# Kernel optimization log

Measured on AMD Instinct MI355X. Metric: run time of the kernel, lower is better.

The kernel has to match this reference:

```python
import jax, jax.numpy as jnp
import numpy as np

N = 100000
E = 1600000


def _sage_conv(x, src, tgt, W_l, b, W_r):
    # PyG SAGEConv (mean aggr): out = lin_l(mean_{j in N(i)} x_j) + lin_r(x_i)
    msg = x[src]                                            # [E, F] gather
    agg = jax.ops.segment_sum(msg, tgt, num_segments=N)     # [N, F]
    deg = jax.ops.segment_sum(jnp.ones((src.shape[0],), x.dtype), tgt, num_segments=N)
    agg = agg / jnp.maximum(deg, 1.0)[:, None]               # mean
    return agg @ W_l + b + x @ W_r


def setup_inputs() -> dict:
    key = jax.random.key(0)
    ks = jax.random.split(key, 16)
    d = {
        "x": jax.random.normal(ks[0], (N, 9), jnp.float32),
        "edge_index": jax.random.randint(ks[1], (2, E), 0, N, jnp.int32).astype(jnp.int64),
        "W1_l": jax.random.normal(ks[2], (9, 128), jnp.float32) / np.sqrt(9),
        "b1": jnp.zeros((128,), jnp.float32),
        "W1_r": jax.random.normal(ks[3], (9, 128), jnp.float32) / np.sqrt(9),
        "W2_l": jax.random.normal(ks[4], (128, 128), jnp.float32) / np.sqrt(128),
        "b2": jnp.zeros((128,), jnp.float32),
        "W2_r": jax.random.normal(ks[5], (128, 128), jnp.float32) / np.sqrt(128),
        "W3_l": jax.random.normal(ks[6], (128, 128), jnp.float32) / np.sqrt(128),
        "b3": jnp.zeros((128,), jnp.float32),
        "W3_r": jax.random.normal(ks[7], (128, 128), jnp.float32) / np.sqrt(128),
        "Wl1": jax.random.normal(ks[8], (128, 128), jnp.float32) / np.sqrt(128),
        "bl1": jnp.zeros((128,), jnp.float32),
        "Wl2": jax.random.normal(ks[9], (128, 64), jnp.float32) / np.sqrt(128),
        "bl2": jnp.zeros((64,), jnp.float32),
        "Wl3": jax.random.normal(ks[10], (64, 3), jnp.float32) / np.sqrt(64),
        "bl3": jnp.zeros((3,), jnp.float32),
    }
    return d


def reference(x, edge_index, W1_l, b1, W1_r, W2_l, b2, W2_r, W3_l, b3, W3_r,
              Wl1, bl1, Wl2, bl2, Wl3, bl3):
    src, tgt = edge_index[0], edge_index[1]
    h = jax.nn.relu(_sage_conv(x, src, tgt, W1_l, b1, W1_r))   # dropout = identity (eval)
    h = jax.nn.relu(_sage_conv(h, src, tgt, W2_l, b2, W2_r))
    h = jax.nn.relu(_sage_conv(h, src, tgt, W3_l, b3, W3_r))
    h = jax.nn.relu(h @ Wl1 + bl1)
    h = jax.nn.relu(h @ Wl2 + bl2)
    h = h @ Wl3 + bl3
    return jax.nn.log_softmax(h, axis=-1)
```

## Files before the change

### kernel.cpp

```cpp
#include <hip/hip_runtime.h>
#include <hip/hip_fp16.h>
#include <stdint.h>

typedef _Float16 f16x8 __attribute__((ext_vector_type(8)));
typedef float f32x4 __attribute__((ext_vector_type(4)));


#define CH 2048
#define MAXNB 1024

__global__ __launch_bounds__(256) void bhist_k(const int* __restrict__ ei,
        int* __restrict__ bh, int E, int shift, int NB, int NBLK) {
    __shared__ int lh[MAXNB];
    for (int b = threadIdx.x; b < NB; b += 256) lh[b] = 0;
    __syncthreads();
    int base = blockIdx.x * CH;
    int end = min(base + CH, E);
    for (int e = base + threadIdx.x; e < end; e += 256) {
        int t = ei[(size_t)E + e];
        atomicAdd(&lh[t >> shift], 1);
    }
    __syncthreads();
    for (int b = threadIdx.x; b < NB; b += 256)
        bh[(size_t)b * NBLK + blockIdx.x] = lh[b];
}

__global__ __launch_bounds__(256) void scan_col_k(int* bh, int* __restrict__ btot,
                                                  int NBLK, int NB) {
    __shared__ int sd[256];
    size_t rowoff = (size_t)blockIdx.x * NBLK;
    int t = threadIdx.x;
    int base = t * 4;
    int v0 = (base + 0 < NBLK) ? bh[rowoff + base + 0] : 0;
    int v1 = (base + 1 < NBLK) ? bh[rowoff + base + 1] : 0;
    int v2 = (base + 2 < NBLK) ? bh[rowoff + base + 2] : 0;
    int v3 = (base + 3 < NBLK) ? bh[rowoff + base + 3] : 0;
    int s = v0 + v1 + v2 + v3;
    sd[t] = s;
    __syncthreads();
    for (int off = 1; off < 256; off <<= 1) {
        int x = (t >= off) ? sd[t - off] : 0;
        __syncthreads();
        sd[t] += x;
        __syncthreads();
    }
    int ex = sd[t] - s;
    if (base + 0 < NBLK) bh[rowoff + base + 0] = ex;
    if (base + 1 < NBLK) bh[rowoff + base + 1] = ex + v0;
    if (base + 2 < NBLK) bh[rowoff + base + 2] = ex + v0 + v1;
    if (base + 3 < NBLK) bh[rowoff + base + 3] = ex + v0 + v1 + v2;
    if (t == 255) btot[blockIdx.x] = sd[255];
}

__global__ void scan_block_k(const int* __restrict__ deg, int* __restrict__ excl,
                             int* __restrict__ bsum, int N) {
    __shared__ int sd[256];
    int t = threadIdx.x;
    int base = blockIdx.x * 1024 + t * 4;
    int v0 = (base + 0 < N) ? deg[base + 0] : 0;
    int v1 = (base + 1 < N) ? deg[base + 1] : 0;
    int v2 = (base + 2 < N) ? deg[base + 2] : 0;
    int v3 = (base + 3 < N) ? deg[base + 3] : 0;
    int s = v0 + v1 + v2 + v3;
    sd[t] = s;
    __syncthreads();
    for (int off = 1; off < 256; off <<= 1) {
        int x = (t >= off) ? sd[t - off] : 0;
        __syncthreads();
        sd[t] += x;
        __syncthreads();
    }
    int incl = sd[t];
    int ex = incl - s;
    if (base + 0 < N) excl[base + 0] = ex;
    if (base + 1 < N) excl[base + 1] = ex + v0;
    if (base + 2 < N) excl[base + 2] = ex + v0 + v1;
    if (base + 3 < N) excl[base + 3] = ex + v0 + v1 + v2;
    if (t == 255) bsum[blockIdx.x] = incl;
}

__global__ __launch_bounds__(256) void bscatter_k(const int* __restrict__ ei,
        const int* __restrict__ bh, const int* __restrict__ bbase,
        int* __restrict__ staged, int E, int shift, int NB, int NBLK) {
    __shared__ int cur[MAXNB];
    for (int b = threadIdx.x; b < NB; b += 256)
        cur[b] = bbase[b] + bh[(size_t)b * NBLK + blockIdx.x];
    __syncthreads();
    int base = blockIdx.x * CH;
    int end = min(base + CH, E);
    int mask = (1 << shift) - 1;
    for (int e = base + threadIdx.x; e < end; e += 256) {
        int s = ei[e];
        int t = ei[(size_t)E + e];
        int p = atomicAdd(&cur[t >> shift], 1);
        staged[p] = s | ((t & mask) << 17);
    }
}

__global__ __launch_bounds__(256) void csrfill_k(const int* __restrict__ staged,
        const int* __restrict__ bbase, int* __restrict__ rs, int* __restrict__ csr,
        int N, int E, int shift, int NB) {
    __shared__ int lh[256];
    __shared__ int sd[256];
    int b = blockIdx.x;
    int tpb = 1 << shift;
    int t0 = b << shift;
    int s0 = bbase[b];
    int s1 = (b == NB - 1) ? E : bbase[b + 1];
    int t = threadIdx.x;
    if (t < tpb) lh[t] = 0;
    __syncthreads();
    for (int e = s0 + t; e < s1; e += 256)
        atomicAdd(&lh[staged[e] >> 17], 1);
    __syncthreads();
    int v = (t < tpb) ? lh[t] : 0;
    sd[t] = v;
    __syncthreads();
    for (int off = 1; off < 256; off <<= 1) {
        int x = (t >= off) ? sd[t - off] : 0;
        __syncthreads();
        sd[t] += x;
        __syncthreads();
    }
    if (t < tpb) {
        int excl = sd[t] - v;
        lh[t] = excl;
        int tg = t0 + t;
        if (tg < N) rs[tg] = s0 + excl;
    }
    if (b == NB - 1 && t == 0) rs[N] = E;
    __syncthreads();
    for (int e = s0 + t; e < s1; e += 256) {
        int w = staged[e];
        int lt = w >> 17;
        int src = w & 0x1FFFF;
        int p = s0 + atomicAdd(&lh[lt], 1);
        csr[p] = src;
    }
}


__global__ void xcast_k(const float* __restrict__ x, __half* __restrict__ x16,
                        int N) {
    int i = blockIdx.x * blockDim.x + threadIdx.x;
    if (i >= N) return;
    const float* xr = x + (size_t)i * 9;
    union { _Float16 h[16]; uint4 u4[2]; } o;
    #pragma unroll
    for (int f = 0; f < 9; ++f) o.h[f] = (_Float16)xr[f];
    #pragma unroll
    for (int f = 9; f < 16; ++f) o.h[f] = (_Float16)0.f;
    uint4* dst = reinterpret_cast<uint4*>(x16 + (size_t)i * 16);
    dst[0] = o.u4[0];
    dst[1] = o.u4[1];
}

__global__ void agg9pack_k(const __half* __restrict__ x16, const int* __restrict__ rs,
                           const int* __restrict__ csr, __half* __restrict__ a32,
                           int N) {
    int i = blockIdx.x * blockDim.x + threadIdx.x;
    if (i >= N) return;
    int s0 = rs[i], s1 = rs[i + 1];
    const uint4* h4 = reinterpret_cast<const uint4*>(x16);
    float a[9];
    #pragma unroll
    for (int f = 0; f < 9; ++f) a[f] = 0.f;
    auto acc9 = [&](int src) {
        uint4 va = h4[(size_t)src * 2];
        unsigned int wb = *reinterpret_cast<const unsigned int*>(
            x16 + (size_t)src * 16 + 8);
        const __half2* p = reinterpret_cast<const __half2*>(&va);
        #pragma unroll
        for (int q = 0; q < 4; ++q) {
            float2 f = __half22float2(p[q]);
            a[q * 2]     += f.x;
            a[q * 2 + 1] += f.y;
        }
        __half2 h8 = *reinterpret_cast<const __half2*>(&wb);
        a[8] += __half22float2(h8).x;
    };
    int j = s0;
    for (; j + 2 <= s1; j += 2) { acc9(csr[j]); acc9(csr[j + 1]); }
    if (j < s1) acc9(csr[j]);
    float inv = (s1 > s0) ? 1.f / (float)(s1 - s0) : 0.f;
    union { _Float16 h[32]; uint4 u4[4]; } o;
    #pragma unroll
    for (int f = 0; f < 9; ++f) o.h[f] = (_Float16)(a[f] * inv);
    const _Float16* sx = reinterpret_cast<const _Float16*>(x16 + (size_t)i * 16);
    #pragma unroll
    for (int f = 0; f < 9; ++f) o.h[9 + f] = sx[f];
    #pragma unroll
    for (int f = 18; f < 32; ++f) o.h[f] = (_Float16)0.f;
    uint4* dst = reinterpret_cast<uint4*>(a32 + (size_t)i * 32);
    #pragma unroll
    for (int q = 0; q < 4; ++q) dst[q] = o.u4[q];
}

__global__ __launch_bounds__(256) void agg128h4_k(const __half* __restrict__ h16,
        const int* __restrict__ rs, const int* __restrict__ csr,
        __half* __restrict__ out, int N) {
    int l16 = threadIdx.x & 15;
    int node = blockIdx.x * 16 + (threadIdx.x >> 4);
    if (node >= N) return;
    int s0 = rs[node], s1 = rs[node + 1];
    const uint4* h4 = reinterpret_cast<const uint4*>(h16);
    float acc[8];
    #pragma unroll
    for (int c = 0; c < 8; ++c) acc[c] = 0.f;
    int j = s0;
    for (; j + 4 <= s1; j += 4) {
        uint4 v[4];
        #pragma unroll
        for (int u = 0; u < 4; ++u)
            v[u] = h4[(size_t)csr[j + u] * 16 + l16];
        #pragma unroll
        for (int u = 0; u < 4; ++u) {
            const __half2* p = reinterpret_cast<const __half2*>(&v[u]);
            #pragma unroll
            for (int q = 0; q < 4; ++q) {
                float2 f = __half22float2(p[q]);
                acc[q * 2]     += f.x;
                acc[q * 2 + 1] += f.y;
            }
        }
    }
    for (; j < s1; ++j) {
        uint4 vv = h4[(size_t)csr[j] * 16 + l16];
        const __half2* p = reinterpret_cast<const __half2*>(&vv);
        #pragma unroll
        for (int q = 0; q < 4; ++q) {
            float2 f = __half22float2(p[q]);
            acc[q * 2]     += f.x;
            acc[q * 2 + 1] += f.y;
        }
    }
    float inv = (s1 > s0) ? 1.f / (float)(s1 - s0) : 0.f;
    __half2 o[4];
    #pragma unroll
    for (int q = 0; q < 4; ++q)
        o[q] = __floats2half2_rn(acc[q * 2] * inv, acc[q * 2 + 1] * inv);
    reinterpret_cast<uint4*>(out)[(size_t)node * 16 + l16] =
        *reinterpret_cast<uint4*>(o);
}


struct WPD { const float* W; _Float16* dst; int K, N; };
struct WPD6 { WPD d[6]; };

__global__ void wpack6_k(WPD6 all) {
    WPD w = all.d[blockIdx.y];
    int idx = blockIdx.x * blockDim.x + threadIdx.x;
    int kcb = w.K / 32;
    int total = (w.N / 16) * kcb * 64;
    if (idx >= total) return;
    int lane = idx & 63;
    int blk = idx >> 6;
    int kb = blk % kcb;
    int nf = blk / kcb;
    int col = nf * 16 + (lane & 15);
    int k0 = kb * 32 + (lane >> 4) * 8;
    f16x8 v;
    #pragma unroll
    for (int j = 0; j < 8; ++j)
        v[j] = (_Float16)w.W[(size_t)(k0 + j) * w.N + col];
    *reinterpret_cast<f16x8*>(w.dst + (size_t)idx * 8) = v;
}

__global__ void wpack1_k(const float* __restrict__ Wl, const float* __restrict__ Wr,
                         _Float16* __restrict__ wpk) {
    int idx = blockIdx.x * blockDim.x + threadIdx.x;
    if (idx >= 8 * 64) return;
    int lane = idx & 63;
    int nf = idx >> 6;
    int col = nf * 16 + (lane & 15);
    int k0 = (lane >> 4) * 8;
    f16x8 v;
    #pragma unroll
    for (int j = 0; j < 8; ++j) {
        int k = k0 + j;
        float w = (k < 9) ? Wl[(size_t)k * 128 + col]
                : (k < 18) ? Wr[(size_t)(k - 9) * 128 + col] : 0.f;
        v[j] = (_Float16)w;
    }
    *reinterpret_cast<f16x8*>(wpk + (size_t)idx * 8) = v;
}

template<int NF, int NS, int KK>
__global__ __launch_bounds__(256) void mfma_lin_k(
        const __half* A1, const __half* A2,
        const _Float16* __restrict__ pk1, const _Float16* __restrict__ pk2,
        const float* __restrict__ bias, __half* C, int M) {
    constexpr int TN = 64 * NF;
    constexpr int KB = KK / 32;
    constexpr int LPR = KK / 8;
    constexpr int RPI = 256 / LPR;
    constexpr int ITER = 64 / RPI;
    __shared__ _Float16 a_lds[NS][64][KK + 8];

    int tid = threadIdx.x;
    int lane = tid & 63;
    int wave = tid >> 6;
    int rb = blockIdx.x * 64;

    const __half* As[2] = {A1, A2};
    #pragma unroll
    for (int s = 0; s < NS; ++s) {
        #pragma unroll
        for (int i = 0; i < ITER; ++i) {
            int row = (tid / LPR) + i * RPI;
            int c = tid % LPR;
            int grow = rb + row;
            uint4 v = make_uint4(0, 0, 0, 0);
            if (grow < M)
                v = reinterpret_cast<const uint4*>(As[s] + (size_t)grow * KK)[c];
            *reinterpret_cast<uint4*>(&a_lds[s][row][c * 8]) = v;
        }
    }

    const _Float16* pks[2] = {pk1, pk2};
    f16x8 bfrag[NS][KB][NF];
    #pragma unroll
    for (int s = 0; s < NS; ++s)
        #pragma unroll
        for (int kb = 0; kb < KB; ++kb)
            #pragma unroll
            for (int n = 0; n < NF; ++n) {
                int nf = wave * NF + n;
                bfrag[s][kb][n] =
                    reinterpret_cast<const f16x8*>(pks[s])[(size_t)(nf * KB + kb) * 64 + lane];
            }

    f32x4 acc[4][NF];
    #pragma unroll
    for (int m = 0; m < 4; ++m)
        #pragma unroll
        for (int n = 0; n < NF; ++n)
            acc[m][n] = (f32x4){0.f, 0.f, 0.f, 0.f};

    __syncthreads();

    #pragma unroll
    for (int s = 0; s < NS; ++s)
        #pragma unroll
        for (int kb = 0; kb < KB; ++kb)
            #pragma unroll
            for (int m = 0; m < 4; ++m) {
                f16x8 a = *reinterpret_cast<const f16x8*>(
                    &a_lds[s][m * 16 + (lane & 15)][kb * 32 + (lane >> 4) * 8]);
                #pragma unroll
                for (int n = 0; n < NF; ++n)
                    acc[m][n] = __builtin_amdgcn_mfma_f32_16x16x32_f16(
                        a, bfrag[s][kb][n], acc[m][n], 0, 0, 0);
            }

    #pragma unroll
    for (int n = 0; n < NF; ++n) {
        int col = wave * NF * 16 + n * 16 + (lane & 15);
        float bv = bias[col];
        #pragma unroll
        for (int m = 0; m < 4; ++m) {
            #pragma unroll
            for (int j = 0; j < 4; ++j) {
                int grow = rb + m * 16 + (lane >> 4) * 4 + j;
                if (grow < M) {
                    float v = fmaxf(acc[m][n][j] + bv, 0.f);
                    C[(size_t)grow * TN + col] = __float2half_rn(v);
                }
            }
        }
    }
}

__global__ __launch_bounds__(256) void mfma_lin_final_k(
        const __half* A1, const _Float16* __restrict__ pk1,
        const float* __restrict__ bias,
        const float* __restrict__ W3, const float* __restrict__ b3,
        float* __restrict__ outp, int M) {
    constexpr int KK = 128;
    __shared__ _Float16 a_lds[64][136];
    __shared__ float smem[64][68];

    int tid = threadIdx.x;
    int lane = tid & 63;
    int wave = tid >> 6;
    int rb = blockIdx.x * 64;

    #pragma unroll
    for (int i = 0; i < 4; ++i) {
        int row = (tid >> 4) + i * 16;
        int grow = rb + row;
        uint4 v = make_uint4(0, 0, 0, 0);
        if (grow < M)
            v = reinterpret_cast<const uint4*>(A1 + (size_t)grow * KK)[tid & 15];
        *reinterpret_cast<uint4*>(&a_lds[row][(tid & 15) * 8]) = v;
    }

    f16x8 bfrag[4];
    #pragma unroll
    for (int kb = 0; kb < 4; ++kb)
        bfrag[kb] = reinterpret_cast<const f16x8*>(pk1)[(size_t)(wave * 4 + kb) * 64 + lane];

    f32x4 acc[4];
    #pragma unroll
    for (int m = 0; m < 4; ++m) acc[m] = (f32x4){0.f, 0.f, 0.f, 0.f};

    __syncthreads();

    #pragma unroll
    for (int kb = 0; kb < 4; ++kb)
        #pragma unroll
        for (int m = 0; m < 4; ++m) {
            f16x8 a = *reinterpret_cast<const f16x8*>(
                &a_lds[m * 16 + (lane & 15)][kb * 32 + (lane >> 4) * 8]);
            acc[m] = __builtin_amdgcn_mfma_f32_16x16x32_f16(a, bfrag[kb], acc[m], 0, 0, 0);
        }

    int col = wave * 16 + (lane & 15);
    float bv = bias[col];
    #pragma unroll
    for (int m = 0; m < 4; ++m)
        #pragma unroll
        for (int j = 0; j < 4; ++j) {
            int row = m * 16 + (lane >> 4) * 4 + j;
            smem[row][col] = fmaxf(acc[m][j] + bv, 0.f);
        }
    __syncthreads();

    if (tid < 64) {
        int grow = rb + tid;
        if (grow < M) {
            float l0 = b3[0], l1 = b3[1], l2 = b3[2];
            #pragma unroll 8
            for (int k = 0; k < 64; ++k) {
                float v = smem[tid][k];
                l0 = fmaf(v, W3[k * 3 + 0], l0);
                l1 = fmaf(v, W3[k * 3 + 1], l1);
                l2 = fmaf(v, W3[k * 3 + 2], l2);
            }
            float mx = fmaxf(l0, fmaxf(l1, l2));
            float e0 = expf(l0 - mx), e1 = expf(l1 - mx), e2 = expf(l2 - mx);
            float lse = logf(e0 + e1 + e2) + mx;
            outp[(size_t)grow * 3 + 0] = l0 - lse;
            outp[(size_t)grow * 3 + 1] = l1 - lse;
            outp[(size_t)grow * 3 + 2] = l2 - lse;
        }
    }
}


extern "C" void kernel_launch(void* const* d_in, const int* in_sizes, int n_in,
                              void* d_out, int out_size, void* d_ws, size_t ws_size,
                              hipStream_t stream) {
    const float* x   = (const float*)d_in[0];
    const int* ei    = (const int*)d_in[1];
    const float* W1l = (const float*)d_in[2];
    const float* b1  = (const float*)d_in[3];
    const float* W1r = (const float*)d_in[4];
    const float* W2l = (const float*)d_in[5];
    const float* b2  = (const float*)d_in[6];
    const float* W2r = (const float*)d_in[7];
    const float* W3l = (const float*)d_in[8];
    const float* b3  = (const float*)d_in[9];
    const float* W3r = (const float*)d_in[10];
    const float* Wl1 = (const float*)d_in[11];
    const float* bl1 = (const float*)d_in[12];
    const float* Wl2 = (const float*)d_in[13];
    const float* bl2 = (const float*)d_in[14];
    const float* Wl3 = (const float*)d_in[15];
    const float* bl3 = (const float*)d_in[16];
    float* out = (float*)d_out;

    const int N = in_sizes[0] / 9;
    const int E = in_sizes[1] / 2;

    char* ws = (char*)d_ws;
    size_t off = 0;
    auto alloc = [&](size_t bytes) -> void* {
        void* p = ws + off;
        off += (bytes + 255) & ~(size_t)255;
        return p;
    };
    __half* h16    = (__half*)alloc((size_t)N * 128 * sizeof(__half));
    __half* agg16  = (__half*)alloc((size_t)N * 128 * sizeof(__half));
    __half* a32    = (__half*)alloc((size_t)N * 32 * sizeof(__half));
    __half* x16    = (__half*)alloc((size_t)N * 16 * sizeof(__half));
    int* rs     = (int*)alloc((size_t)(N + 1) * sizeof(int));
    int* csr    = (int*)alloc((size_t)E * sizeof(int));
    int* staged = (int*)alloc((size_t)E * sizeof(int));
    _Float16* wpk1  = (_Float16*)alloc(32 * 128 * sizeof(_Float16));
    _Float16* wpk2l = (_Float16*)alloc(128 * 128 * sizeof(_Float16));
    _Float16* wpk2r = (_Float16*)alloc(128 * 128 * sizeof(_Float16));
    _Float16* wpk3l = (_Float16*)alloc(128 * 128 * sizeof(_Float16));
    _Float16* wpk3r = (_Float16*)alloc(128 * 128 * sizeof(_Float16));
    _Float16* wpkl1 = (_Float16*)alloc(128 * 128 * sizeof(_Float16));
    _Float16* wpkl2 = (_Float16*)alloc(128 * 64 * sizeof(_Float16));
    (void)ws_size; (void)n_in; (void)out_size;

    int shift = 7;
    while ((((size_t)N + ((size_t)1 << shift) - 1) >> shift) > MAXNB) ++shift;
    const int NB = (N + (1 << shift) - 1) >> shift;
    const int NBLK = (E + CH - 1) / CH;
    int* bh    = (int*)alloc((size_t)NB * NBLK * sizeof(int));
    int* btot  = (int*)alloc((size_t)NB * sizeof(int));
    int* bbase = (int*)alloc((size_t)(NB + 1) * sizeof(int));
    int* bsum  = (int*)alloc(64 * sizeof(int));

    WPD6 wp;
    wp.d[0] = {W2l, wpk2l, 128, 128};
    wp.d[1] = {W2r, wpk2r, 128, 128};
    wp.d[2] = {W3l, wpk3l, 128, 128};
    wp.d[3] = {W3r, wpk3r, 128, 128};
    wp.d[4] = {Wl1, wpkl1, 128, 128};
    wp.d[5] = {Wl2, wpkl2, 128, 64};
    wpack6_k<<<dim3(8, 6), 256, 0, stream>>>(wp);
    wpack1_k<<<2, 256, 0, stream>>>(W1l, W1r, wpk1);
    xcast_k<<<(N + 255) / 256, 256, 0, stream>>>(x, x16, N);

    bhist_k<<<NBLK, 256, 0, stream>>>(ei, bh, E, shift, NB, NBLK);
    scan_col_k<<<NB, 256, 0, stream>>>(bh, btot, NBLK, NB);
    scan_block_k<<<1, 256, 0, stream>>>(btot, bbase, bsum, NB);
    bscatter_k<<<NBLK, 256, 0, stream>>>(ei, bh, bbase, staged, E, shift, NB, NBLK);
    csrfill_k<<<NB, 256, 0, stream>>>(staged, bbase, rs, csr, N, E, shift, NB);

    const int gemm_grid = (N + 63) / 64;
    const int agg_grid = (N + 15) / 16;

    agg9pack_k<<<(N + 255) / 256, 256, 0, stream>>>(x16, rs, csr, a32, N);
    mfma_lin_k<2, 1, 32><<<gemm_grid, 256, 0, stream>>>(
        a32, nullptr, wpk1, nullptr, b1, h16, N);

    agg128h4_k<<<agg_grid, 256, 0, stream>>>(h16, rs, csr, agg16, N);
    mfma_lin_k<2, 2, 128><<<gemm_grid, 256, 0, stream>>>(
        agg16, h16, wpk2l, wpk2r, b2, h16, N);

    agg128h4_k<<<agg_grid, 256, 0, stream>>>(h16, rs, csr, agg16, N);
    mfma_lin_k<2, 2, 128><<<gemm_grid, 256, 0, stream>>>(
        agg16, h16, wpk3l, wpk3r, b3, h16, N);

    mfma_lin_k<2, 1, 128><<<gemm_grid, 256, 0, stream>>>(
        h16, nullptr, wpkl1, nullptr, bl1, h16, N);
    mfma_lin_final_k<<<gemm_grid, 256, 0, stream>>>(
        h16, wpkl2, bl2, Wl3, bl3, out, N);
}
```

Baseline: 289.6 us.

## Fuse neighbor mean aggregation into SAGE layer GEMM kernel

Replaces the separate 128-wide gather-mean kernel and the following MFMA GEMM with a single kernel. Each block aggregates neighbors for its 64 rows directly into LDS, loads its own rows into a second LDS buffer, then runs both weight products from LDS. This removes the write and re-read of the intermediate aggregate buffer and one launch per layer. Because a node's output now depends on other blocks' inputs, it ping-pongs between two feature buffers, and each block now does gather and GEMM in sequence, which can lower occupancy and overlap.

```diff
diff --git a/kernel.cpp b/kernel.cpp
--- a/kernel.cpp
+++ b/kernel.cpp
@@ -194,53 +194,6 @@
     uint4* dst = reinterpret_cast<uint4*>(a32 + (size_t)i * 32);
     #pragma unroll
     for (int q = 0; q < 4; ++q) dst[q] = o.u4[q];
-}
-
-__global__ __launch_bounds__(256) void agg128h4_k(const __half* __restrict__ h16,
-        const int* __restrict__ rs, const int* __restrict__ csr,
-        __half* __restrict__ out, int N) {
-    int l16 = threadIdx.x & 15;
-    int node = blockIdx.x * 16 + (threadIdx.x >> 4);
-    if (node >= N) return;
-    int s0 = rs[node], s1 = rs[node + 1];
-    const uint4* h4 = reinterpret_cast<const uint4*>(h16);
-    float acc[8];
-    #pragma unroll
-    for (int c = 0; c < 8; ++c) acc[c] = 0.f;
-    int j = s0;
-    for (; j + 4 <= s1; j += 4) {
-        uint4 v[4];
-        #pragma unroll
-        for (int u = 0; u < 4; ++u)
-            v[u] = h4[(size_t)csr[j + u] * 16 + l16];
-        #pragma unroll
-        for (int u = 0; u < 4; ++u) {
-            const __half2* p = reinterpret_cast<const __half2*>(&v[u]);
-            #pragma unroll
-            for (int q = 0; q < 4; ++q) {
-                float2 f = __half22float2(p[q]);
-                acc[q * 2]     += f.x;
-                acc[q * 2 + 1] += f.y;
-            }
-        }
-    }
-    for (; j < s1; ++j) {
-        uint4 vv = h4[(size_t)csr[j] * 16 + l16];
-        const __half2* p = reinterpret_cast<const __half2*>(&vv);
-        #pragma unroll
-        for (int q = 0; q < 4; ++q) {
-            float2 f = __half22float2(p[q]);
-            acc[q * 2]     += f.x;
-            acc[q * 2 + 1] += f.y;
-        }
-    }
-    float inv = (s1 > s0) ? 1.f / (float)(s1 - s0) : 0.f;
-    __half2 o[4];
-    #pragma unroll
-    for (int q = 0; q < 4; ++q)
-        o[q] = __floats2half2_rn(acc[q * 2] * inv, acc[q * 2 + 1] * inv);
-    reinterpret_cast<uint4*>(out)[(size_t)node * 16 + l16] =
-        *reinterpret_cast<uint4*>(o);
 }
 
 
@@ -365,6 +318,130 @@
                 if (grow < M) {
                     float v = fmaxf(acc[m][n][j] + bv, 0.f);
                     C[(size_t)grow * TN + col] = __float2half_rn(v);
+                }
+            }
+        }
+    }
+}
+
+__global__ __launch_bounds__(256) void agg_gemm_k(
+        const __half* __restrict__ hin,
+        const int* __restrict__ rs, const int* __restrict__ csr,
+        const _Float16* __restrict__ pkl, const _Float16* __restrict__ pkr,
+        const float* __restrict__ bias, __half* __restrict__ hout, int M) {
+    constexpr int KK = 128;
+    __shared__ _Float16 a_lds[2][64][KK + 8];
+
+    int tid = threadIdx.x;
+    int lane = tid & 63;
+    int wave = tid >> 6;
+    int rb = blockIdx.x * 64;
+    int l16 = lane & 15;
+
+    #pragma unroll
+    for (int i = 0; i < 4; ++i) {
+        int row = (tid >> 4) + i * 16;
+        int grow = rb + row;
+        uint4 v = make_uint4(0, 0, 0, 0);
+        if (grow < M)
+            v = reinterpret_cast<const uint4*>(hin + (size_t)grow * KK)[l16];
+        *reinterpret_cast<uint4*>(&a_lds[1][row][l16 * 8]) = v;
+    }
+
+    const uint4* h4 = reinterpret_cast<const uint4*>(hin);
+    #pragma unroll
+    for (int it = 0; it < 4; ++it) {
+        int row = wave * 16 + it * 4 + (lane >> 4);
+        int node = rb + row;
+        float acc[8];
+        #pragma unroll
+        for (int c = 0; c < 8; ++c) acc[c] = 0.f;
+        int s0 = 0, s1 = 0;
+        if (node < M) { s0 = rs[node]; s1 = rs[node + 1]; }
+        int j = s0;
+        for (; j + 4 <= s1; j += 4) {
+            uint4 v[4];
+            #pragma unroll
+            for (int u = 0; u < 4; ++u)
+                v[u] = h4[(size_t)csr[j + u] * 16 + l16];
+            #pragma unroll
+            for (int u = 0; u < 4; ++u) {
+                const __half2* p = reinterpret_cast<const __half2*>(&v[u]);
+                #pragma unroll
+                for (int q = 0; q < 4; ++q) {
+                    float2 f = __half22float2(p[q]);
+                    acc[q * 2]     += f.x;
+                    acc[q * 2 + 1] += f.y;
+                }
+            }
+        }
+        for (; j < s1; ++j) {
+            uint4 vv = h4[(size_t)csr[j] * 16 + l16];
+            const __half2* p = reinterpret_cast<const __half2*>(&vv);
+            #pragma unroll
+            for (int q = 0; q < 4; ++q) {
+                float2 f = __half22float2(p[q]);
+                acc[q * 2]     += f.x;
+                acc[q * 2 + 1] += f.y;
+            }
+        }
+        float inv = (s1 > s0) ? 1.f / (float)(s1 - s0) : 0.f;
+        __half2 o[4];
+        #pragma unroll
+        for (int q = 0; q < 4; ++q)
+            o[q] = __floats2half2_rn(acc[q * 2] * inv, acc[q * 2 + 1] * inv);
+        *reinterpret_cast<uint4*>(&a_lds[0][row][l16 * 8]) =
+            *reinterpret_cast<uint4*>(o);
+    }
+
+    const _Float16* pks[2] = {pkl, pkr};
+    f16x8 bfrag[2][4][2];
+    #pragma unroll
+    for (int s = 0; s < 2; ++s)
+        #pragma unroll
+        for (int kb = 0; kb < 4; ++kb)
+            #pragma unroll
+            for (int n = 0; n < 2; ++n) {
+                int nf = wave * 2 + n;
+                bfrag[s][kb][n] =
+                    reinterpret_cast<const f16x8*>(pks[s])[(size_t)(nf * 4 + kb) * 64 + lane];
+            }
+
+    f32x4 acc[4][2];
+    #pragma unroll
+    for (int m = 0; m < 4; ++m)
+        #pragma unroll
+        for (int n = 0; n < 2; ++n)
+            acc[m][n] = (f32x4){0.f, 0.f, 0.f, 0.f};
+
+    __syncthreads();
+
+    #pragma unroll
+    for (int s = 0; s < 2; ++s)
+        #pragma unroll
+        for (int kb = 0; kb < 4; ++kb)
+            #pragma unroll
+            for (int m = 0; m < 4; ++m) {
+                f16x8 a = *reinterpret_cast<const f16x8*>(
+                    &a_lds[s][m * 16 + (lane & 15)][kb * 32 + (lane >> 4) * 8]);
+                #pragma unroll
+                for (int n = 0; n < 2; ++n)
+                    acc[m][n] = __builtin_amdgcn_mfma_f32_16x16x32_f16(
+                        a, bfrag[s][kb][n], acc[m][n], 0, 0, 0);
+            }
+
+    #pragma unroll
+    for (int n = 0; n < 2; ++n) {
+        int col = wave * 32 + n * 16 + (lane & 15);
+        float bv = bias[col];
+        #pragma unroll
+        for (int m = 0; m < 4; ++m) {
+            #pragma unroll
+            for (int j = 0; j < 4; ++j) {
+                int grow = rb + m * 16 + (lane >> 4) * 4 + j;
+                if (grow < M) {
+                    float v = fmaxf(acc[m][n][j] + bv, 0.f);
+                    hout[(size_t)grow * 128 + col] = __float2half_rn(v);
                 }
             }
         }
@@ -481,7 +558,7 @@
         return p;
     };
     __half* h16    = (__half*)alloc((size_t)N * 128 * sizeof(__half));
-    __half* agg16  = (__half*)alloc((size_t)N * 128 * sizeof(__half));
+    __half* hb     = (__half*)alloc((size_t)N * 128 * sizeof(__half));
     __half* a32    = (__half*)alloc((size_t)N * 32 * sizeof(__half));
     __half* x16    = (__half*)alloc((size_t)N * 16 * sizeof(__half));
     int* rs     = (int*)alloc((size_t)(N + 1) * sizeof(int));
@@ -523,19 +600,16 @@
     csrfill_k<<<NB, 256, 0, stream>>>(staged, bbase, rs, csr, N, E, shift, NB);
 
     const int gemm_grid = (N + 63) / 64;
-    const int agg_grid = (N + 15) / 16;
 
     agg9pack_k<<<(N + 255) / 256, 256, 0, stream>>>(x16, rs, csr, a32, N);
     mfma_lin_k<2, 1, 32><<<gemm_grid, 256, 0, stream>>>(
         a32, nullptr, wpk1, nullptr, b1, h16, N);
 
-    agg128h4_k<<<agg_grid, 256, 0, stream>>>(h16, rs, csr, agg16, N);
-    mfma_lin_k<2, 2, 128><<<gemm_grid, 256, 0, stream>>>(
-        agg16, h16, wpk2l, wpk2r, b2, h16, N);
-
-    agg128h4_k<<<agg_grid, 256, 0, stream>>>(h16, rs, csr, agg16, N);
-    mfma_lin_k<2, 2, 128><<<gemm_grid, 256, 0, stream>>>(
-        agg16, h16, wpk3l, wpk3r, b3, h16, N);
+    agg_gemm_k<<<gemm_grid, 256, 0, stream>>>(
+        h16, rs, csr, wpk2l, wpk2r, b2, hb, N);
+
+    agg_gemm_k<<<gemm_grid, 256, 0, stream>>>(
+        hb, rs, csr, wpk3l, wpk3r, b3, h16, N);
 
     mfma_lin_k<2, 1, 128><<<gemm_grid, 256, 0, stream>>>(
         h16, nullptr, wpkl1, nullptr, bl1, h16, N);
```

After: 293.0 us. Within noise of the previous version (+1.2%).
